# Kernel tuning notes

Measured on AMD Instinct MI355X. Metric: run time of the kernel, lower is better.

## Reference

```python
import jax, jax.numpy as jnp
import numpy as np

N, D = 8192, 64
TAU = 0.5
ALPHA1 = 0.5
ALPHA2 = 0.5
EPS = 1e-8
EDGE_P = 0.002  # sparse thresholded-attention graph


def setup_inputs() -> dict:
    key = jax.random.key(0)
    k1, k2, k3, k4 = jax.random.split(key, 4)
    z = jax.random.normal(k1, (N, D), dtype=jnp.float32)
    z_aug = jax.random.normal(k2, (N, D), dtype=jnp.float32)
    # binary adjacency masks (float, as in the torch code), zero diagonal
    adj = (jax.random.uniform(k3, (N, N)) < EDGE_P).astype(jnp.float32)
    adj = adj * (1.0 - jnp.eye(N, dtype=jnp.float32))
    adj_aug = (jax.random.uniform(k4, (N, N)) < EDGE_P).astype(jnp.float32)
    adj_aug = adj_aug * (1.0 - jnp.eye(N, dtype=jnp.float32))
    return {"z": z, "z_aug": z_aug, "adj": adj, "adj_aug": adj_aug}


def _l2norm(x):
    # F.normalize(x, dim=1): x / max(||x||, eps) with eps=1e-12
    n = jnp.sqrt(jnp.sum(x * x, axis=1, keepdims=True))
    return x / jnp.maximum(n, 1e-12)


def _contrastive_loss(z, z_aug, adj, tau):
    zn = _l2norm(z)            # [N, D]
    zan = _l2norm(z_aug)       # [N, D]
    intra = jnp.exp(zn @ zn.T / tau)    # [N, N]
    inter = jnp.exp(zn @ zan.T / tau)   # [N, N]
    inter_diag = jnp.diagonal(inter)
    intra_diag = jnp.diagonal(intra)
    positive = inter_diag + jnp.sum(intra * adj, axis=1) + jnp.sum(inter * adj, axis=1)
    denominator = jnp.sum(intra, axis=1) + jnp.sum(inter, axis=1) - intra_diag
    loss = positive / (denominator + EPS)
    adj_count = jnp.sum(adj, axis=1) * 2.0 + 1.0
    loss = jnp.log(loss + EPS) / adj_count
    return -jnp.mean(loss)


def reference(z, z_aug, adj, adj_aug):
    loss = ALPHA1 * _contrastive_loss(z, z_aug, adj, TAU)
    loss = loss + ALPHA2 * _contrastive_loss(z_aug, z, adj_aug, TAU)
    return loss
```

## Files before the change

kernel.cpp:

```cpp
#include <hip/hip_runtime.h>
#include <hip/hip_bf16.h>

#define NROWS 8192
#define DDIM 64
#define GROWS 16384
#define BROWS 256
#define BCOLS 256
#define CH 16
#define NCH 16

typedef __attribute__((ext_vector_type(8))) short short8v;
typedef __attribute__((ext_vector_type(4))) float f32x4;

#define K2CONST 2.885390081777927f
#define EPSC 1e-8f

#define AS1 __attribute__((address_space(1)))
#define AS3 __attribute__((address_space(3)))

__global__ __launch_bounds__(256) void k_normalize(
    const float* __restrict__ z, const float* __restrict__ za,
    __hip_bfloat16* __restrict__ Pb, __hip_bfloat16* __restrict__ Pk,
    float* __restrict__ dI1, float* __restrict__ dI2, float* __restrict__ dX) {
  int wid = (blockIdx.x * blockDim.x + threadIdx.x) >> 6;
  int lane = threadIdx.x & 63;
  if (wid >= NROWS) return;
  float x = z[wid * DDIM + lane];
  float y = za[wid * DDIM + lane];
  float sx = x * x, sy = y * y, sxy = x * y;
  for (int m = 1; m < 64; m <<= 1) {
    sx  += __shfl_xor(sx, m);
    sy  += __shfl_xor(sy, m);
    sxy += __shfl_xor(sxy, m);
  }
  float inx = 1.0f / fmaxf(sqrtf(sx), 1e-12f);
  float iny = 1.0f / fmaxf(sqrtf(sy), 1e-12f);
  float xn = x * inx, yn = y * iny;
  Pb[wid * DDIM + lane] = __float2bfloat16(xn);
  Pb[(NROWS + wid) * DDIM + lane] = __float2bfloat16(yn);
  Pk[wid * DDIM + lane] = __float2bfloat16(xn * K2CONST);
  Pk[(NROWS + wid) * DDIM + lane] = __float2bfloat16(yn * K2CONST);
  if (lane == 0) {
    dI1[wid] = expf(sx * inx * inx * 2.0f);
    dI2[wid] = expf(sy * iny * iny * 2.0f);
    dX[wid]  = expf(sxy * iny * inx * 2.0f);
  }
}

__global__ __launch_bounds__(256) void k_fused(
    const __hip_bfloat16* __restrict__ Pb, const __hip_bfloat16* __restrict__ Pk,
    const float* __restrict__ adj, const float* __restrict__ adj_aug,
    float* __restrict__ sD, float* __restrict__ sM, float* __restrict__ cnt) {
  __shared__ __align__(16) float ladj[4][CH][BCOLS];
  __shared__ __align__(16) __hip_bfloat16 lpk[4][CH][DDIM];

  const int tid = threadIdx.x;
  const int w = tid >> 6, lane = tid & 63;
  const int r_in = lane & 15, kq = lane >> 4;
  const int rb = blockIdx.x >> 5;
  const int cb = blockIdx.x & 31;
  const int grow0 = rb * BROWS;
  const int c0 = cb * BCOLS;
  const float* ADJ = (rb < 32) ? adj : adj_aug;
  const int arow0 = (rb & 31) * BROWS;

  const short8v* P8 = reinterpret_cast<const short8v*>(Pb);
  short8v bA0[4], bA1[4], bB0[4], bB1[4];
#pragma unroll
  for (int t = 0; t < 4; t++) {
    int col = c0 + w * 64 + t * 16 + r_in;
    bA0[t] = P8[col * 8 + kq];
    bA1[t] = P8[col * 8 + kq + 4];
    bB0[t] = P8[(col + NROWS) * 8 + kq];
    bB1[t] = P8[(col + NROWS) * 8 + kq + 4];
  }

#define STAGE(CC, SS) {                                                        \
    _Pragma("unroll")                                                          \
    for (int q = 0; q < 4; q++) {                                              \
      int r_ = w * 4 + q;                                                      \
      const float* gsrc_ = ADJ + (size_t)(arow0 + (CC) * CH + r_) * NROWS      \
                           + c0 + lane * 4;                                    \
      __builtin_amdgcn_global_load_lds(                                        \
          (const AS1 unsigned int*)gsrc_,                                      \
          (AS3 unsigned int*)&ladj[SS][r_][0], 16, 0, 0);                      \
    }                                                                          \
    if (w < 2) {                                                               \
      const __hip_bfloat16* psrc_ = Pk                                         \
          + (size_t)(grow0 + (CC) * CH + w * 8) * DDIM + lane * 8;             \
      __builtin_amdgcn_global_load_lds(                                        \
          (const AS1 unsigned int*)psrc_,                                      \
          (AS3 unsigned int*)&lpk[SS][w * 8][0], 16, 0, 0);                    \
    }                                                                          \
  }

  STAGE(0, 0); STAGE(1, 1); STAGE(2, 2);

  for (int k = 0; k < NCH; k++) {
    STAGE((k + 3) & 15, (k + 3) & 3);
    if (w < 2) asm volatile("s_waitcnt vmcnt(15)" ::: "memory");
    else       asm volatile("s_waitcnt vmcnt(12)" ::: "memory");
    __builtin_amdgcn_s_barrier();

    const int ss = k & 3;
    short8v a0 = *(const short8v*)&lpk[ss][r_in][kq * 8];
    short8v a1 = *(const short8v*)&lpk[ss][r_in][kq * 8 + 32];
    float dsum = 0.f, msum = 0.f, csum = 0.f;
#pragma unroll
    for (int t = 0; t < 4; t++) {
      f32x4 av = *(const f32x4*)&ladj[ss][r_in][w * 64 + t * 16 + kq * 4];
      f32x4 g0 = (f32x4){0.f, 0.f, 0.f, 0.f};
      g0 = __builtin_amdgcn_mfma_f32_16x16x32_bf16(bA0[t], a0, g0, 0, 0, 0);
      g0 = __builtin_amdgcn_mfma_f32_16x16x32_bf16(bA1[t], a1, g0, 0, 0, 0);
      f32x4 g1 = (f32x4){0.f, 0.f, 0.f, 0.f};
      g1 = __builtin_amdgcn_mfma_f32_16x16x32_bf16(bB0[t], a0, g1, 0, 0, 0);
      g1 = __builtin_amdgcn_mfma_f32_16x16x32_bf16(bB1[t], a1, g1, 0, 0, 0);
#pragma unroll
      for (int c = 0; c < 4; c++) {
        float e = __builtin_amdgcn_exp2f(g0[c]) + __builtin_amdgcn_exp2f(g1[c]);
        dsum += e;
        msum += av[c] * e;
        csum += av[c];
      }
    }
    dsum += __shfl_xor(dsum, 16); dsum += __shfl_xor(dsum, 32);
    msum += __shfl_xor(msum, 16); msum += __shfl_xor(msum, 32);
    csum += __shfl_xor(csum, 16); csum += __shfl_xor(csum, 32);
    if (lane < 16) {
      int row = grow0 + k * CH + r_in;
      atomicAdd(&sD[row], dsum);
      atomicAdd(&sM[row], msum);
      atomicAdd(&cnt[row], csum);
    }
    __builtin_amdgcn_s_barrier();
  }
#undef STAGE
}

__global__ __launch_bounds__(256) void k_final_partial(
    const float* __restrict__ sD, const float* __restrict__ sM,
    const float* __restrict__ dI1, const float* __restrict__ dI2,
    const float* __restrict__ dX,
    const float* __restrict__ cnt, float* __restrict__ acc) {
  int i = blockIdx.x * blockDim.x + threadIdx.x;
  float pos1 = dX[i] + sM[i];
  float den1 = sD[i] - dI1[i];
  float l1 = logf(pos1 / (den1 + EPSC) + EPSC) / (2.0f * cnt[i] + 1.0f);
  float pos2 = dX[i] + sM[NROWS + i];
  float den2 = sD[NROWS + i] - dI2[i];
  float l2 = logf(pos2 / (den2 + EPSC) + EPSC) / (2.0f * cnt[NROWS + i] + 1.0f);
  float local = l1 + l2;
#pragma unroll
  for (int m = 1; m < 64; m <<= 1) local += __shfl_xor(local, m);
  if ((threadIdx.x & 63) == 0) atomicAdd(acc, local);
}

__global__ void k_finalize(const float* __restrict__ acc, float* __restrict__ out) {
  out[0] = -acc[0] * (0.5f / (float)NROWS);
}

extern "C" void kernel_launch(void* const* d_in, const int* in_sizes, int n_in,
                              void* d_out, int out_size, void* d_ws, size_t ws_size,
                              hipStream_t stream) {
  const float* z       = (const float*)d_in[0];
  const float* za      = (const float*)d_in[1];
  const float* adj     = (const float*)d_in[2];
  const float* adj_aug = (const float*)d_in[3];

  float* ws = (float*)d_ws;
  __hip_bfloat16* Pb = (__hip_bfloat16*)ws;
  __hip_bfloat16* Pk = (__hip_bfloat16*)(ws + 524288);
  float* Z0   = ws + 1048576;
  float* sD   = Z0;
  float* sM   = Z0 + 16384;
  float* cnt  = Z0 + 32768;
  float* acc  = Z0 + 49152;
  float* dI1  = Z0 + 49153;
  float* dI2  = dI1 + 8192;
  float* dX   = dI2 + 8192;

  hipMemsetAsync(Z0, 0, 49153 * sizeof(float), stream);

  k_normalize<<<2048, 256, 0, stream>>>(z, za, Pb, Pk, dI1, dI2, dX);
  k_fused<<<2048, 256, 0, stream>>>(Pb, Pk, adj, adj_aug, sD, sM, cnt);
  k_final_partial<<<32, 256, 0, stream>>>(sD, sM, dI1, dI2, dX, cnt, acc);
  k_finalize<<<1, 1, 0, stream>>>(acc, (float*)d_out);
}
```

Measured before the change: 153.4 us.

## Give each wave private LDS buffers and drop block-wide barriers in fused kernel

Each wave now stages its own 64-column slice of the adjacency tile and its own copy of the scaled row block into a private triple-buffered LDS region. Because no data is shared across waves, the two s_barriers per chunk are removed and synchronisation relies only on per-wave vmcnt waits. The adjacency is read in a per-lane layout matching the MFMA output. The cost is that every wave loads the Pk rows redundantly, and the hand-tuned vmcnt counts must exactly match the outstanding loads and atomics.

```diff
diff --git a/kernel.cpp b/kernel.cpp
--- a/kernel.cpp
+++ b/kernel.cpp
@@ -3,7 +3,6 @@
 
 #define NROWS 8192
 #define DDIM 64
-#define GROWS 16384
 #define BROWS 256
 #define BCOLS 256
 #define CH 16
@@ -51,8 +50,7 @@
     const __hip_bfloat16* __restrict__ Pb, const __hip_bfloat16* __restrict__ Pk,
     const float* __restrict__ adj, const float* __restrict__ adj_aug,
     float* __restrict__ sD, float* __restrict__ sM, float* __restrict__ cnt) {
-  __shared__ __align__(16) float ladj[4][CH][BCOLS];
-  __shared__ __align__(16) __hip_bfloat16 lpk[4][CH][DDIM];
+  __shared__ __align__(16) char lds[4][3][6144];
 
   const int tid = threadIdx.x;
   const int w = tid >> 6, lane = tid & 63;
@@ -60,7 +58,7 @@
   const int rb = blockIdx.x >> 5;
   const int cb = blockIdx.x & 31;
   const int grow0 = rb * BROWS;
-  const int c0 = cb * BCOLS;
+  const int c0 = cb * BCOLS + w * 64;
   const float* ADJ = (rb < 32) ? adj : adj_aug;
   const int arow0 = (rb & 31) * BROWS;
 
@@ -68,72 +66,75 @@
   short8v bA0[4], bA1[4], bB0[4], bB1[4];
 #pragma unroll
   for (int t = 0; t < 4; t++) {
-    int col = c0 + w * 64 + t * 16 + r_in;
+    int col = c0 + t * 16 + r_in;
     bA0[t] = P8[col * 8 + kq];
     bA1[t] = P8[col * 8 + kq + 4];
     bB0[t] = P8[(col + NROWS) * 8 + kq];
     bB1[t] = P8[(col + NROWS) * 8 + kq + 4];
   }
+  asm volatile("s_waitcnt vmcnt(0)" ::: "memory");
 
-#define STAGE(CC, SS) {                                                        \
+  const float* asrc = ADJ + (size_t)(arow0 + r_in) * NROWS + c0 + kq * 4;
+  const __hip_bfloat16* psrc = Pk + (size_t)(grow0 + r_in) * DDIM + kq * 8;
+
+#define STAGE(K) {                                                             \
+    char* db_ = &lds[w][(K) % 3][0];                                           \
     _Pragma("unroll")                                                          \
-    for (int q = 0; q < 4; q++) {                                              \
-      int r_ = w * 4 + q;                                                      \
-      const float* gsrc_ = ADJ + (size_t)(arow0 + (CC) * CH + r_) * NROWS      \
-                           + c0 + lane * 4;                                    \
+    for (int u = 0; u < 4; u++)                                                \
       __builtin_amdgcn_global_load_lds(                                        \
-          (const AS1 unsigned int*)gsrc_,                                      \
-          (AS3 unsigned int*)&ladj[SS][r_][0], 16, 0, 0);                      \
-    }                                                                          \
-    if (w < 2) {                                                               \
-      const __hip_bfloat16* psrc_ = Pk                                         \
-          + (size_t)(grow0 + (CC) * CH + w * 8) * DDIM + lane * 8;             \
+          (const AS1 unsigned int*)(asrc + (size_t)(K) * (CH * NROWS) + u*16), \
+          (AS3 unsigned int*)(db_ + u * 1024), 16, 0, 0);                      \
+    _Pragma("unroll")                                                          \
+    for (int h = 0; h < 2; h++)                                                \
       __builtin_amdgcn_global_load_lds(                                        \
-          (const AS1 unsigned int*)psrc_,                                      \
-          (AS3 unsigned int*)&lpk[SS][w * 8][0], 16, 0, 0);                    \
-    }                                                                          \
+          (const AS1 unsigned int*)(psrc + (size_t)(K) * (CH * DDIM) + h*32),  \
+          (AS3 unsigned int*)(db_ + 4096 + h * 1024), 16, 0, 0);               \
   }
 
-  STAGE(0, 0); STAGE(1, 1); STAGE(2, 2);
+#define CHUNK(K, WAITSTR, DOSTAGE) {                                           \
+    asm volatile(WAITSTR ::: "memory");                                        \
+    const char* sb_ = &lds[w][(K) % 3][0];                                     \
+    short8v a0 = *(const short8v*)(sb_ + 4096 + (kq * 16 + r_in) * 16);        \
+    short8v a1 = *(const short8v*)(sb_ + 5120 + (kq * 16 + r_in) * 16);        \
+    float dsum = 0.f, msum = 0.f, csum = 0.f;                                  \
+    _Pragma("unroll")                                                          \
+    for (int t = 0; t < 4; t++) {                                              \
+      f32x4 av = *(const f32x4*)(sb_ + t * 1024 + kq * 256 + r_in * 16);       \
+      f32x4 g0 = (f32x4){0.f, 0.f, 0.f, 0.f};                                  \
+      g0 = __builtin_amdgcn_mfma_f32_16x16x32_bf16(bA0[t], a0, g0, 0, 0, 0);   \
+      g0 = __builtin_amdgcn_mfma_f32_16x16x32_bf16(bA1[t], a1, g0, 0, 0, 0);   \
+      f32x4 g1 = (f32x4){0.f, 0.f, 0.f, 0.f};                                  \
+      g1 = __builtin_amdgcn_mfma_f32_16x16x32_bf16(bB0[t], a0, g1, 0, 0, 0);   \
+      g1 = __builtin_amdgcn_mfma_f32_16x16x32_bf16(bB1[t], a1, g1, 0, 0, 0);   \
+      _Pragma("unroll")                                                        \
+      for (int c = 0; c < 4; c++) {                                            \
+        float e = __builtin_amdgcn_exp2f(g0[c]) + __builtin_amdgcn_exp2f(g1[c]);\
+        dsum += e; msum += av[c] * e; csum += av[c];                           \
+      }                                                                        \
+    }                                                                          \
+    dsum += __shfl_xor(dsum, 16); dsum += __shfl_xor(dsum, 32);                \
+    msum += __shfl_xor(msum, 16); msum += __shfl_xor(msum, 32);                \
+    csum += __shfl_xor(csum, 16); csum += __shfl_xor(csum, 32);                \
+    if (lane < 16) {                                                           \
+      int row_ = grow0 + (K) * CH + r_in;                                      \
+      atomicAdd(&sD[row_], dsum);                                              \
+      atomicAdd(&sM[row_], msum);                                              \
+      atomicAdd(&cnt[row_], csum);                                             \
+    }                                                                          \
+    if (DOSTAGE) STAGE((K) + 3);                                               \
+  }
 
-  for (int k = 0; k < NCH; k++) {
-    STAGE((k + 3) & 15, (k + 3) & 3);
-    if (w < 2) asm volatile("s_waitcnt vmcnt(15)" ::: "memory");
-    else       asm volatile("s_waitcnt vmcnt(12)" ::: "memory");
-    __builtin_amdgcn_s_barrier();
+  STAGE(0); STAGE(1); STAGE(2);
 
-    const int ss = k & 3;
-    short8v a0 = *(const short8v*)&lpk[ss][r_in][kq * 8];
-    short8v a1 = *(const short8v*)&lpk[ss][r_in][kq * 8 + 32];
-    float dsum = 0.f, msum = 0.f, csum = 0.f;
-#pragma unroll
-    for (int t = 0; t < 4; t++) {
-      f32x4 av = *(const f32x4*)&ladj[ss][r_in][w * 64 + t * 16 + kq * 4];
-      f32x4 g0 = (f32x4){0.f, 0.f, 0.f, 0.f};
-      g0 = __builtin_amdgcn_mfma_f32_16x16x32_bf16(bA0[t], a0, g0, 0, 0, 0);
-      g0 = __builtin_amdgcn_mfma_f32_16x16x32_bf16(bA1[t], a1, g0, 0, 0, 0);
-      f32x4 g1 = (f32x4){0.f, 0.f, 0.f, 0.f};
-      g1 = __builtin_amdgcn_mfma_f32_16x16x32_bf16(bB0[t], a0, g1, 0, 0, 0);
-      g1 = __builtin_amdgcn_mfma_f32_16x16x32_bf16(bB1[t], a1, g1, 0, 0, 0);
-#pragma unroll
-      for (int c = 0; c < 4; c++) {
-        float e = __builtin_amdgcn_exp2f(g0[c]) + __builtin_amdgcn_exp2f(g1[c]);
-        dsum += e;
-        msum += av[c] * e;
-        csum += av[c];
-      }
-    }
-    dsum += __shfl_xor(dsum, 16); dsum += __shfl_xor(dsum, 32);
-    msum += __shfl_xor(msum, 16); msum += __shfl_xor(msum, 32);
-    csum += __shfl_xor(csum, 16); csum += __shfl_xor(csum, 32);
-    if (lane < 16) {
-      int row = grow0 + k * CH + r_in;
-      atomicAdd(&sD[row], dsum);
-      atomicAdd(&sM[row], msum);
-      atomicAdd(&cnt[row], csum);
-    }
-    __builtin_amdgcn_s_barrier();
+  CHUNK(0, "s_waitcnt vmcnt(12)", true);
+  CHUNK(1, "s_waitcnt vmcnt(15)", true);
+  for (int k = 2; k <= 12; k++) {
+    CHUNK(k, "s_waitcnt vmcnt(18)", true);
   }
+  CHUNK(13, "s_waitcnt vmcnt(18)", false);
+  CHUNK(14, "s_waitcnt vmcnt(12)", false);
+  CHUNK(15, "s_waitcnt vmcnt(6)",  false);
+#undef CHUNK
 #undef STAGE
 }
 
```

Result: faster. 149.7 us (-2.4%).
